# Performance work log

Measured on AMD Instinct MI355X. Metric: run time of the kernel, lower is better.

The kernel has to match this reference:

```python
import jax, jax.numpy as jnp
import numpy as np

B, L, D = 2, 2048, 768
HID = 32           # saliency gate hidden dim
WINDOWS = (8, 32)  # sorted window sizes
CLAMP_MIN, CLAMP_MAX = 0.05, 0.95
SCALE = 1.0 / np.sqrt(D)  # memory_dim == d_model


def setup_inputs() -> dict:
    key = jax.random.key(0)
    ks = jax.random.split(key, 16)
    s = 0.02
    return {
        "hidden_states": jax.random.normal(ks[0], (B, L, D), jnp.float32),
        "saliency_scores": jax.random.uniform(ks[1], (B, L), jnp.float32),
        # SaliencyGate MLP: Linear(1->HID), SiLU, Linear(HID->D)
        "gw1": jax.random.normal(ks[2], (HID, 1), jnp.float32) * s,
        "gb1": jnp.zeros((HID,), jnp.float32),
        "gw2": jax.random.normal(ks[3], (D, HID), jnp.float32) * s,
        "gb2": jnp.zeros((D,), jnp.float32),
        # SelectiveMemory projections
        "wq": jax.random.normal(ks[4], (D, D), jnp.float32) * s,
        "bq": jnp.zeros((D,), jnp.float32),
        "wk": jax.random.normal(ks[5], (D, D), jnp.float32) * s,
        "bk": jnp.zeros((D,), jnp.float32),
        "wv": jax.random.normal(ks[6], (D, D), jnp.float32) * s,
        "bv": jnp.zeros((D,), jnp.float32),
        "wo": jax.random.normal(ks[7], (D, D), jnp.float32) * s,
        "bo": jnp.zeros((D,), jnp.float32),
    }


def _forward(hidden_states, saliency_scores, gw1, gb1, gw2, gb2,
             wq, bq, wk, bk, wv, bv, wo, bo):
    # ---- SaliencyGate: scalar score -> MLP -> sigmoid gate -> clamp ----
    s = saliency_scores[..., None]                          # (b, l, 1)
    h1 = jax.nn.silu(s @ gw1.T + gb1)                       # (b, l, HID)
    gates = jax.nn.sigmoid(h1 @ gw2.T + gb2)                # (b, l, D)
    gates = jnp.clip(gates, CLAMP_MIN, CLAMP_MAX)
    h = hidden_states * gates

    # ---- SelectiveMemory: multi-window local attention ----
    q = h @ wq.T + bq                                       # (b, l, D)
    k = h @ wk.T + bk
    v = h @ wv.T + bv
    # Torch pads hidden_states with zeros before k/v projection; linear of a
    # zero row equals the bias, so padded key/value rows are exactly bk / bv.
    contexts = []
    for w in WINDOWS:
        kp = jnp.concatenate(
            [jnp.broadcast_to(bk, (B, w - 1, D)), k], axis=1)  # (b, l+w-1, D)
        vp = jnp.concatenate(
            [jnp.broadcast_to(bv, (B, w - 1, D)), v], axis=1)
        idx = jnp.arange(L)[:, None] + jnp.arange(w)[None, :]  # (l, w)
        kw = kp[:, idx]                                        # (b, l, w, D)
        vw = vp[:, idx]
        scores = jnp.einsum('bld,blwd->blw', q, kw) * SCALE
        attn = jax.nn.softmax(scores, axis=-1)
        contexts.append(jnp.einsum('blw,blwd->bld', attn, vw))
    merged = (contexts[0] + contexts[1]) * 0.5 if len(contexts) > 1 else contexts[0]
    return h + merged @ wo.T + bo


def reference(hidden_states, saliency_scores, gw1, gb1, gw2, gb2,
              wq, bq, wk, bk, wv, bv, wo, bo):
    return _forward(hidden_states, saliency_scores, gw1, gb1, gw2, gb2,
                    wq, bq, wk, bk, wv, bv, wo, bo)
```

## Files before the change

kernel.cpp:

```cpp
#include <hip/hip_runtime.h>
#include <hip/hip_bf16.h>
#include <stdint.h>

#define Bb 2
#define Ll 2048
#define Dd 768
#define HID 32
#define BL (Bb*Ll)
#define KPAD 32
#define KROWS (KPAD+Ll+16)

typedef __hip_bfloat16 bf16;
typedef __attribute__((ext_vector_type(8))) short short8;
typedef __attribute__((ext_vector_type(4))) short short4s;
typedef __attribute__((ext_vector_type(4))) float floatx4;

__device__ __forceinline__ float b2f(short u) {
    union { float f; unsigned i; } x; x.i = ((unsigned)(unsigned short)u) << 16; return x.f;
}
__device__ __forceinline__ bf16 f2b(float x) { return __float2bfloat16(x); }
__device__ __forceinline__ short f2bs(float x) {
    bf16 t = __float2bfloat16(x);
    union { bf16 h; short s; } u; u.h = t; return u.s;
}

typedef __attribute__((address_space(1))) const unsigned int guint;
typedef __attribute__((address_space(3))) unsigned int luint;
__device__ __forceinline__ void gload16(const bf16* g, bf16* l) {
    __builtin_amdgcn_global_load_lds((guint*)g, (luint*)l, 16, 0, 0);
}

#define CONV_BLOCKS 2304
#define KP_BLOCKS   (Bb*48)
#define VT_BLOCKS   ((Bb*Dd*48)/256)
#define TR_BLOCKS   96
__global__ void prep_kernel(const float* __restrict__ wq, const float* __restrict__ wk,
                            const float* __restrict__ wv, const float* __restrict__ wo,
                            const float* __restrict__ bk, const float* __restrict__ bv,
                            const float* __restrict__ gw2,
                            bf16* __restrict__ wout, bf16* __restrict__ kp, bf16* __restrict__ vT,
                            float* __restrict__ gw2T) {
    int bx = blockIdx.x;
    if (bx < CONV_BLOCKS) {
        int idx = bx * 256 + threadIdx.x;
        const int per = Dd * Dd / 4;
        int w = idx / per, r = idx % per;
        const float* src = (w == 0) ? wq : (w == 1) ? wk : (w == 2) ? wv : wo;
        float4 v = reinterpret_cast<const float4*>(src)[r];
        bf16* o = wout + (size_t)w * Dd * Dd + (size_t)r * 4;
        o[0] = f2b(v.x); o[1] = f2b(v.y); o[2] = f2b(v.z); o[3] = f2b(v.w);
    } else if (bx < CONV_BLOCKS + KP_BLOCKS) {
        int pb = bx - CONV_BLOCKS;
        int b = pb / 48, c = pb % 48;
        int row = (c < 32) ? c : (KPAD + Ll + (c - 32));
        size_t base = ((size_t)b * KROWS + row) * Dd;
        for (int i = threadIdx.x; i < Dd; i += 256)
            kp[base + i] = (c < 32) ? f2b(bk[i]) : f2b(0.f);
    } else if (bx < CONV_BLOCKS + KP_BLOCKS + VT_BLOCKS) {
        int o = (bx - CONV_BLOCKS - KP_BLOCKS) * 256 + threadIdx.x;
        int b = o / (Dd * 48); int rem = o - b * Dd * 48;
        int n = rem / 48, c = rem % 48;
        int col = (c < 32) ? c : (KPAD + Ll + (c - 32));
        vT[((size_t)b * Dd + n) * KROWS + col] = (c < 32) ? f2b(bv[n]) : f2b(0.f);
    } else {
        int o = (bx - CONV_BLOCKS - KP_BLOCKS - VT_BLOCKS) * 256 + threadIdx.x;
        int j = o / Dd, d = o - j * Dd;
        gw2T[o] = gw2[d * HID + j];
    }
}

__global__ __launch_bounds__(256) void gate_kernel(
        const float* __restrict__ hidden, const float* __restrict__ sal,
        const float* __restrict__ gw1, const float* __restrict__ gb1,
        const float* __restrict__ gw2T, const float* __restrict__ gb2,
        bf16* __restrict__ h_b) {
    __shared__ float h1s[8][HID];
    int row0 = blockIdx.x * 8;
    int t = threadIdx.x;
    {
        int rr = t >> 5, j = t & 31;
        float s = sal[row0 + rr];
        float x = s * gw1[j] + gb1[j];
        h1s[rr][j] = x / (1.f + __expf(-x));
    }
    __syncthreads();
#pragma unroll
    for (int dl = 0; dl < 3; ++dl) {
        int d = t + dl * 256;
        float base = gb2[d];
        float acc[8];
#pragma unroll
        for (int rr = 0; rr < 8; ++rr) acc[rr] = base;
#pragma unroll
        for (int j = 0; j < HID; ++j) {
            float wj = gw2T[j * Dd + d];
#pragma unroll
            for (int rr = 0; rr < 8; ++rr) acc[rr] += h1s[rr][j] * wj;
        }
#pragma unroll
        for (int rr = 0; rr < 8; ++rr) {
            float g = 1.f / (1.f + __expf(-acc[rr]));
            g = fminf(fmaxf(g, 0.05f), 0.95f);
            size_t off = (size_t)(row0 + rr) * Dd + d;
            h_b[off] = f2b(hidden[off] * g);
        }
    }
}

template<int NF>
__device__ __forceinline__ void gemm_core(const bf16* __restrict__ Ag, const bf16* __restrict__ Wg,
                                          int m0, int n0, bf16* As, bf16* Bs,
                                          floatx4 (&acc)[4][NF]) {
    const int tid  = threadIdx.x;
    const int wave = tid >> 6, lane = tid & 63;
    const int lrow = lane & 15, koff = (lane >> 4) * 8;
    const int wm = (wave >> 1) * 64, wn = (wave & 1) * (NF * 16);
    const char* Asb = (const char*)As;
    const char* Bsb = (const char*)Bs;

    for (int k0 = 0; k0 < Dd; k0 += 64) {
#pragma unroll
        for (int c = 0; c < 4; ++c) {
            int p = tid * 16 + c * 4096;
            int r = p >> 7;
            int o = (p & 127) ^ ((r & 7) << 4);
            gload16(Ag + (size_t)(m0 + r) * Dd + k0 + (o >> 1),
                    As + (wave * 1024 + c * 4096) / 2);
        }
#pragma unroll
        for (int c = 0; c < NF; ++c) {
            int p = tid * 16 + c * 4096;
            int r = p >> 7;
            int o = (p & 127) ^ ((r & 7) << 4);
            gload16(Wg + (size_t)(n0 + r) * Dd + k0 + (o >> 1),
                    Bs + (wave * 1024 + c * 4096) / 2);
        }
        __syncthreads();
#pragma unroll
        for (int kk = 0; kk < 64; kk += 32) {
            short8 a[4], b[NF];
#pragma unroll
            for (int i = 0; i < 4; ++i) {
                int row = wm + i * 16 + lrow;
                int byt = (row << 7) + (((kk + koff) * 2) ^ ((row & 7) << 4));
                a[i] = *reinterpret_cast<const short8*>(Asb + byt);
            }
#pragma unroll
            for (int j = 0; j < NF; ++j) {
                int row = wn + j * 16 + lrow;
                int byt = (row << 7) + (((kk + koff) * 2) ^ ((row & 7) << 4));
                b[j] = *reinterpret_cast<const short8*>(Bsb + byt);
            }
#pragma unroll
            for (int i = 0; i < 4; ++i)
#pragma unroll
                for (int j = 0; j < NF; ++j)
                    acc[i][j] = __builtin_amdgcn_mfma_f32_16x16x32_bf16(a[i], b[j], acc[i][j], 0, 0, 0);
        }
        __syncthreads();
    }
}

__global__ __launch_bounds__(256) void gemm_qkv(
        const bf16* __restrict__ A, const bf16* __restrict__ W3,
        const float* __restrict__ bq, const float* __restrict__ bk, const float* __restrict__ bv,
        bf16* __restrict__ qo, bf16* __restrict__ kp, bf16* __restrict__ vT) {
    __shared__ bf16 As[128 * 64];
    __shared__ bf16 Bs[128 * 64];
    int bid = blockIdx.x;
    int xcd = bid & 7, idx = bid >> 3;
    int mtile = (xcd >> 1) * 8 + (idx & 7);
    int ntile = (xcd & 1) * 9 + (idx >> 3);
    int tgt = ntile / 6;
    int n0 = (ntile % 6) * 128;
    int m0 = mtile * 128;
    const bf16* W = W3 + (size_t)tgt * Dd * Dd;
    const float* bias = (tgt == 0) ? bq : (tgt == 1) ? bk : bv;

    floatx4 acc[4][4] = {};
    gemm_core<4>(A, W, m0, n0, As, Bs, acc);

    int wave = threadIdx.x >> 6, lane = threadIdx.x & 63;
    int wm = (wave >> 1) * 64, wn = (wave & 1) * 64;
    int crow = (lane >> 4) * 4, ccol = lane & 15;
#pragma unroll
    for (int i = 0; i < 4; ++i)
#pragma unroll
        for (int j = 0; j < 4; ++j) {
            int n = n0 + wn + j * 16 + ccol;
            float bb = bias[n];
            int m = m0 + wm + i * 16 + crow;
            int b_ = m >> 11, l = m & 2047;
            if (tgt == 2) {
                short4s pk;
#pragma unroll
                for (int rr = 0; rr < 4; ++rr) pk[rr] = f2bs(acc[i][j][rr] + bb);
                *reinterpret_cast<short4s*>(vT + ((size_t)b_ * Dd + n) * KROWS + KPAD + l) = pk;
            } else {
#pragma unroll
                for (int rr = 0; rr < 4; ++rr) {
                    size_t orow = (tgt == 0) ? (size_t)(m + rr)
                                             : ((size_t)b_ * KROWS + KPAD + l + rr);
                    bf16* out = (tgt == 0) ? qo : kp;
                    out[orow * Dd + n] = f2b(acc[i][j][rr] + bb);
                }
            }
        }
}

__global__ __launch_bounds__(256) void gemm_out(
        const bf16* __restrict__ A, const bf16* __restrict__ W,
        const float* __restrict__ bias, const bf16* __restrict__ addend,
        float* __restrict__ out) {
    __shared__ bf16 As[128 * 64];
    __shared__ bf16 Bs[64 * 64];
    int bid = blockIdx.x;
    int xcd = bid & 7, idx = bid >> 3;
    int mtile = (xcd >> 1) * 8 + (idx & 7);
    int ntile = (xcd & 1) * 6 + (idx >> 3);
    int n0 = ntile * 64, m0 = mtile * 128;

    floatx4 acc[4][2] = {};
    gemm_core<2>(A, W, m0, n0, As, Bs, acc);

    int wave = threadIdx.x >> 6, lane = threadIdx.x & 63;
    int wm = (wave >> 1) * 64, wn = (wave & 1) * 32;
    int crow = (lane >> 4) * 4, ccol = lane & 15;
#pragma unroll
    for (int i = 0; i < 4; ++i)
#pragma unroll
        for (int j = 0; j < 2; ++j) {
            int n = n0 + wn + j * 16 + ccol;
            float bb = bias[n];
#pragma unroll
            for (int rr = 0; rr < 4; ++rr) {
                int m = m0 + wm + i * 16 + crow + rr;
                size_t o = (size_t)m * Dd + n;
                out[o] = acc[i][j][rr] + bb + b2f(*(const short*)(addend + o));
            }
        }
}

__global__ __launch_bounds__(64) void attn_kernel(
        const bf16* __restrict__ q, const bf16* __restrict__ kp, const bf16* __restrict__ vT,
        bf16* __restrict__ merged) {
    __shared__ bf16 wlds[16 * 64];
    const int lane = threadIdx.x;
    const int bid = blockIdx.x;
    const int g = (bid & 7) * 32 + (bid >> 3);
    const int b = g >> 7, L0 = (g & 127) * 16;
    const int lrow = lane & 15, koff = (lane >> 4) * 8;
    const int crow = (lane >> 4) * 4, ccol = lane & 15;
    const float scale = 0.03608439182435161f;

    const bf16* qbase = q  + ((size_t)(b * Ll + L0 + lrow)) * Dd + koff;
    const bf16* kbase = kp + ((size_t)b * KROWS + L0 + lrow) * Dd + koff;
    floatx4 s[4] = {};
    for (int ks = 0; ks < 24; ++ks) {
        short8 a = *reinterpret_cast<const short8*>(qbase + ks * 32);
#pragma unroll
        for (int f = 0; f < 4; ++f) {
            short8 bb = *reinterpret_cast<const short8*>(kbase + (size_t)f * 16 * Dd + ks * 32);
            s[f] = __builtin_amdgcn_mfma_f32_16x16x32_bf16(a, bb, s[f], 0, 0, 0);
        }
    }

#pragma unroll
    for (int rr = 0; rr < 4; ++rr) {
        int r = crow + rr;
        float z[4], e[4];
#pragma unroll
        for (int f = 0; f < 4; ++f) {
            int j = f * 16 + ccol;
            bool valid = (j >= r + 1) && (j <= r + 32);
            z[f] = valid ? s[f][rr] * scale : -3.0e38f;
        }
        float m = fmaxf(fmaxf(z[0], z[1]), fmaxf(z[2], z[3]));
#pragma unroll
        for (int off = 1; off < 16; off <<= 1) m = fmaxf(m, __shfl_xor(m, off));
        float S32 = 0.f, S8 = 0.f;
#pragma unroll
        for (int f = 0; f < 4; ++f) {
            e[f] = __expf(z[f] - m);
            S32 += e[f];
            int j = f * 16 + ccol;
            S8 += ((j >= r + 25) && (j <= r + 32)) ? e[f] : 0.f;
        }
#pragma unroll
        for (int off = 1; off < 16; off <<= 1) {
            S32 += __shfl_xor(S32, off);
            S8  += __shfl_xor(S8, off);
        }
        float i32 = 0.5f / S32, i8 = 0.5f / S8;
#pragma unroll
        for (int f = 0; f < 4; ++f) {
            int j = f * 16 + ccol;
            float w = e[f] * i32 + (((j >= r + 25) && (j <= r + 32)) ? e[f] * i8 : 0.f);
            int byt = ((r * 64 + j) * 2) ^ ((r & 7) << 4);
            *reinterpret_cast<bf16*>(reinterpret_cast<char*>(wlds) + byt) = f2b(w);
        }
    }
    __syncthreads();

    short8 wa[2];
#pragma unroll
    for (int ks = 0; ks < 2; ++ks) {
        int byt = ((lrow * 64 + ks * 32 + koff) * 2) ^ ((lrow & 7) << 4);
        wa[ks] = *reinterpret_cast<const short8*>(reinterpret_cast<const char*>(wlds) + byt);
    }
    const bf16* vbase = vT + (size_t)b * Dd * KROWS + L0;
    bf16* obase = merged + ((size_t)(b * Ll + L0 + ccol)) * Dd;
    for (int c = 0; c < 6; ++c) {
#pragma unroll
        for (int fn = 0; fn < 8; ++fn) {
            int nr = c * 128 + fn * 16;
            floatx4 acc = {};
#pragma unroll
            for (int ks = 0; ks < 2; ++ks) {
                short8 bb = *reinterpret_cast<const short8*>(vbase + (size_t)(nr + lrow) * KROWS + ks * 32 + koff);
                acc = __builtin_amdgcn_mfma_f32_16x16x32_bf16(bb, wa[ks], acc, 0, 0, 0);
            }
            short4s pk;
#pragma unroll
            for (int rr = 0; rr < 4; ++rr) pk[rr] = f2bs(acc[rr]);
            *reinterpret_cast<short4s*>(obase + nr + crow) = pk;
        }
    }
}

extern "C" void kernel_launch(void* const* d_in, const int* in_sizes, int n_in,
                              void* d_out, int out_size, void* d_ws, size_t ws_size,
                              hipStream_t stream) {
    const float* hidden = (const float*)d_in[0];
    const float* sal    = (const float*)d_in[1];
    const float* gw1    = (const float*)d_in[2];
    const float* gb1    = (const float*)d_in[3];
    const float* gw2    = (const float*)d_in[4];
    const float* gb2    = (const float*)d_in[5];
    const float* wq     = (const float*)d_in[6];
    const float* bq     = (const float*)d_in[7];
    const float* wk     = (const float*)d_in[8];
    const float* bk     = (const float*)d_in[9];
    const float* wv     = (const float*)d_in[10];
    const float* bv     = (const float*)d_in[11];
    const float* wo     = (const float*)d_in[12];
    const float* bo     = (const float*)d_in[13];
    float* out = (float*)d_out;

    const size_t nBL  = (size_t)BL * Dd;
    const size_t nPad = (size_t)Bb * KROWS * Dd;
    char* p = (char*)d_ws;
    bf16* h_b = (bf16*)p; p += nBL * 2;
    bf16* q_b = (bf16*)p; p += nBL * 2;
    bf16* kpd = (bf16*)p; p += nPad * 2;
    bf16* vT  = (bf16*)p; p += nPad * 2;
    bf16* m_b = (bf16*)p; p += nBL * 2;
    bf16* w_b = (bf16*)p; p += (size_t)4 * Dd * Dd * 2;
    float* g2T = (float*)p; p += (size_t)HID * Dd * 4;

    prep_kernel<<<dim3(CONV_BLOCKS + KP_BLOCKS + VT_BLOCKS + TR_BLOCKS), 256, 0, stream>>>(
        wq, wk, wv, wo, bk, bv, gw2, w_b, kpd, vT, g2T);
    gate_kernel<<<dim3(BL / 8), 256, 0, stream>>>(hidden, sal, gw1, gb1, g2T, gb2, h_b);
    gemm_qkv<<<dim3(576), 256, 0, stream>>>(h_b, w_b, bq, bk, bv, q_b, kpd, vT);
    attn_kernel<<<dim3(256), 64, 0, stream>>>(q_b, kpd, vT, m_b);
    gemm_out<<<dim3(384), 256, 0, stream>>>(m_b, w_b + (size_t)3 * Dd * Dd, bo, h_b, out);
}
```

Measured before the change: 84.26 us.

## Fuse prep and gate kernels, widen QKV GEMM K-tile to 128

Merges the weight-conversion/padding prep kernel with the saliency gate kernel into one launch. Each gate block now transposes gw2 into shared memory as bf16 itself, so the separate transpose pass and the global gw2T buffer are gone. The QKV GEMM uses a 128-wide K tile, which halves its loop iterations and barriers but doubles its shared memory, and both GEMMs get a two-blocks-per-CU launch bound. Every gate block re-reads all of gw2 and uses a 49KB shared array, which can lower occupancy for the whole fused kernel, including the cheap prep blocks.

```diff
diff --git a/kernel.cpp b/kernel.cpp
--- a/kernel.cpp
+++ b/kernel.cpp
@@ -30,84 +30,88 @@
     __builtin_amdgcn_global_load_lds((guint*)g, (luint*)l, 16, 0, 0);
 }
 
-#define CONV_BLOCKS 2304
-#define KP_BLOCKS   (Bb*48)
-#define VT_BLOCKS   ((Bb*Dd*48)/256)
-#define TR_BLOCKS   96
-__global__ void prep_kernel(const float* __restrict__ wq, const float* __restrict__ wk,
-                            const float* __restrict__ wv, const float* __restrict__ wo,
-                            const float* __restrict__ bk, const float* __restrict__ bv,
-                            const float* __restrict__ gw2,
-                            bf16* __restrict__ wout, bf16* __restrict__ kp, bf16* __restrict__ vT,
-                            float* __restrict__ gw2T) {
-    int bx = blockIdx.x;
-    if (bx < CONV_BLOCKS) {
-        int idx = bx * 256 + threadIdx.x;
+#define CONV_VB 2304
+#define KP_VB   (Bb*48)
+#define VT_VB   ((Bb*Dd*48)/256)
+#define PREP_VB (CONV_VB+KP_VB+VT_VB)
+#define GATE_VB (BL/8)
+__global__ __launch_bounds__(256) void prep_gate_kernel(
+        const float* __restrict__ wq, const float* __restrict__ wk,
+        const float* __restrict__ wv, const float* __restrict__ wo,
+        const float* __restrict__ bk, const float* __restrict__ bv,
+        const float* __restrict__ hidden, const float* __restrict__ sal,
+        const float* __restrict__ gw1, const float* __restrict__ gb1,
+        const float* __restrict__ gw2, const float* __restrict__ gb2,
+        bf16* __restrict__ wout, bf16* __restrict__ kp, bf16* __restrict__ vT,
+        bf16* __restrict__ h_b) {
+    __shared__ bf16 g2t[32 * 770];
+    __shared__ float h1s[8][HID];
+    int bx = blockIdx.x, tid = threadIdx.x;
+    if (bx < CONV_VB) {
+        int idx = bx * 256 + tid;
         const int per = Dd * Dd / 4;
         int w = idx / per, r = idx % per;
         const float* src = (w == 0) ? wq : (w == 1) ? wk : (w == 2) ? wv : wo;
         float4 v = reinterpret_cast<const float4*>(src)[r];
         bf16* o = wout + (size_t)w * Dd * Dd + (size_t)r * 4;
         o[0] = f2b(v.x); o[1] = f2b(v.y); o[2] = f2b(v.z); o[3] = f2b(v.w);
-    } else if (bx < CONV_BLOCKS + KP_BLOCKS) {
-        int pb = bx - CONV_BLOCKS;
+    } else if (bx < CONV_VB + KP_VB) {
+        int pb = bx - CONV_VB;
         int b = pb / 48, c = pb % 48;
         int row = (c < 32) ? c : (KPAD + Ll + (c - 32));
         size_t base = ((size_t)b * KROWS + row) * Dd;
-        for (int i = threadIdx.x; i < Dd; i += 256)
+        for (int i = tid; i < Dd; i += 256)
             kp[base + i] = (c < 32) ? f2b(bk[i]) : f2b(0.f);
-    } else if (bx < CONV_BLOCKS + KP_BLOCKS + VT_BLOCKS) {
-        int o = (bx - CONV_BLOCKS - KP_BLOCKS) * 256 + threadIdx.x;
+    } else if (bx < PREP_VB) {
+        int o = (bx - CONV_VB - KP_VB) * 256 + tid;
         int b = o / (Dd * 48); int rem = o - b * Dd * 48;
         int n = rem / 48, c = rem % 48;
         int col = (c < 32) ? c : (KPAD + Ll + (c - 32));
         vT[((size_t)b * Dd + n) * KROWS + col] = (c < 32) ? f2b(bv[n]) : f2b(0.f);
     } else {
-        int o = (bx - CONV_BLOCKS - KP_BLOCKS - VT_BLOCKS) * 256 + threadIdx.x;
-        int j = o / Dd, d = o - j * Dd;
-        gw2T[o] = gw2[d * HID + j];
-    }
-}
-
-__global__ __launch_bounds__(256) void gate_kernel(
-        const float* __restrict__ hidden, const float* __restrict__ sal,
-        const float* __restrict__ gw1, const float* __restrict__ gb1,
-        const float* __restrict__ gw2T, const float* __restrict__ gb2,
-        bf16* __restrict__ h_b) {
-    __shared__ float h1s[8][HID];
-    int row0 = blockIdx.x * 8;
-    int t = threadIdx.x;
-    {
-        int rr = t >> 5, j = t & 31;
-        float s = sal[row0 + rr];
-        float x = s * gw1[j] + gb1[j];
-        h1s[rr][j] = x / (1.f + __expf(-x));
-    }
-    __syncthreads();
-#pragma unroll
-    for (int dl = 0; dl < 3; ++dl) {
-        int d = t + dl * 256;
-        float base = gb2[d];
-        float acc[8];
-#pragma unroll
-        for (int rr = 0; rr < 8; ++rr) acc[rr] = base;
-#pragma unroll
-        for (int j = 0; j < HID; ++j) {
-            float wj = gw2T[j * Dd + d];
-#pragma unroll
-            for (int rr = 0; rr < 8; ++rr) acc[rr] += h1s[rr][j] * wj;
-        }
-#pragma unroll
-        for (int rr = 0; rr < 8; ++rr) {
-            float g = 1.f / (1.f + __expf(-acc[rr]));
-            g = fminf(fmaxf(g, 0.05f), 0.95f);
-            size_t off = (size_t)(row0 + rr) * Dd + d;
-            h_b[off] = f2b(hidden[off] * g);
-        }
-    }
-}
-
-template<int NF>
+        int row0 = (bx - PREP_VB) * 8;
+#pragma unroll
+        for (int k2 = 0; k2 < 24; ++k2) {
+            int o4 = tid + k2 * 256;
+            float4 v = reinterpret_cast<const float4*>(gw2)[o4];
+            int d = o4 >> 3, j = (o4 & 7) * 4;
+            g2t[(j + 0) * 770 + d] = f2b(v.x);
+            g2t[(j + 1) * 770 + d] = f2b(v.y);
+            g2t[(j + 2) * 770 + d] = f2b(v.z);
+            g2t[(j + 3) * 770 + d] = f2b(v.w);
+        }
+        {
+            int rr = tid >> 5, j = tid & 31;
+            float s = sal[row0 + rr];
+            float x = s * gw1[j] + gb1[j];
+            h1s[rr][j] = x / (1.f + __expf(-x));
+        }
+        __syncthreads();
+#pragma unroll
+        for (int dl = 0; dl < 3; ++dl) {
+            int d = tid + dl * 256;
+            float base = gb2[d];
+            float acc[8];
+#pragma unroll
+            for (int rr = 0; rr < 8; ++rr) acc[rr] = base;
+#pragma unroll
+            for (int j = 0; j < HID; ++j) {
+                float wj = b2f(*(const short*)&g2t[j * 770 + d]);
+#pragma unroll
+                for (int rr = 0; rr < 8; ++rr) acc[rr] += h1s[rr][j] * wj;
+            }
+#pragma unroll
+            for (int rr = 0; rr < 8; ++rr) {
+                float g = 1.f / (1.f + __expf(-acc[rr]));
+                g = fminf(fmaxf(g, 0.05f), 0.95f);
+                size_t off = (size_t)(row0 + rr) * Dd + d;
+                h_b[off] = f2b(hidden[off] * g);
+            }
+        }
+    }
+}
+
+template<int NF, int BK>
 __device__ __forceinline__ void gemm_core(const bf16* __restrict__ Ag, const bf16* __restrict__ Wg,
                                           int m0, int n0, bf16* As, bf16* Bs,
                                           floatx4 (&acc)[4][NF]) {
@@ -115,40 +119,41 @@
     const int wave = tid >> 6, lane = tid & 63;
     const int lrow = lane & 15, koff = (lane >> 4) * 8;
     const int wm = (wave >> 1) * 64, wn = (wave & 1) * (NF * 16);
+    const int RS = BK * 2;
     const char* Asb = (const char*)As;
     const char* Bsb = (const char*)Bs;
 
-    for (int k0 = 0; k0 < Dd; k0 += 64) {
-#pragma unroll
-        for (int c = 0; c < 4; ++c) {
+    for (int k0 = 0; k0 < Dd; k0 += BK) {
+#pragma unroll
+        for (int c = 0; c < BK / 16; ++c) {
             int p = tid * 16 + c * 4096;
-            int r = p >> 7;
-            int o = (p & 127) ^ ((r & 7) << 4);
+            int r = p / RS;
+            int o = (p % RS) ^ ((r & 7) << 4);
             gload16(Ag + (size_t)(m0 + r) * Dd + k0 + (o >> 1),
                     As + (wave * 1024 + c * 4096) / 2);
         }
 #pragma unroll
-        for (int c = 0; c < NF; ++c) {
+        for (int c = 0; c < NF * BK / 64; ++c) {
             int p = tid * 16 + c * 4096;
-            int r = p >> 7;
-            int o = (p & 127) ^ ((r & 7) << 4);
+            int r = p / RS;
+            int o = (p % RS) ^ ((r & 7) << 4);
             gload16(Wg + (size_t)(n0 + r) * Dd + k0 + (o >> 1),
                     Bs + (wave * 1024 + c * 4096) / 2);
         }
         __syncthreads();
 #pragma unroll
-        for (int kk = 0; kk < 64; kk += 32) {
+        for (int kk = 0; kk < BK; kk += 32) {
             short8 a[4], b[NF];
 #pragma unroll
             for (int i = 0; i < 4; ++i) {
                 int row = wm + i * 16 + lrow;
-                int byt = (row << 7) + (((kk + koff) * 2) ^ ((row & 7) << 4));
+                int byt = row * RS + (((kk + koff) * 2) ^ ((row & 7) << 4));
                 a[i] = *reinterpret_cast<const short8*>(Asb + byt);
             }
 #pragma unroll
             for (int j = 0; j < NF; ++j) {
                 int row = wn + j * 16 + lrow;
-                int byt = (row << 7) + (((kk + koff) * 2) ^ ((row & 7) << 4));
+                int byt = row * RS + (((kk + koff) * 2) ^ ((row & 7) << 4));
                 b[j] = *reinterpret_cast<const short8*>(Bsb + byt);
             }
 #pragma unroll
@@ -161,12 +166,12 @@
     }
 }
 
-__global__ __launch_bounds__(256) void gemm_qkv(
+__global__ __launch_bounds__(256, 2) void gemm_qkv(
         const bf16* __restrict__ A, const bf16* __restrict__ W3,
         const float* __restrict__ bq, const float* __restrict__ bk, const float* __restrict__ bv,
         bf16* __restrict__ qo, bf16* __restrict__ kp, bf16* __restrict__ vT) {
-    __shared__ bf16 As[128 * 64];
-    __shared__ bf16 Bs[128 * 64];
+    __shared__ bf16 As[128 * 128];
+    __shared__ bf16 Bs[128 * 128];
     int bid = blockIdx.x;
     int xcd = bid & 7, idx = bid >> 3;
     int mtile = (xcd >> 1) * 8 + (idx & 7);
@@ -178,7 +183,7 @@
     const float* bias = (tgt == 0) ? bq : (tgt == 1) ? bk : bv;
 
     floatx4 acc[4][4] = {};
-    gemm_core<4>(A, W, m0, n0, As, Bs, acc);
+    gemm_core<4, 128>(A, W, m0, n0, As, Bs, acc);
 
     int wave = threadIdx.x >> 6, lane = threadIdx.x & 63;
     int wm = (wave >> 1) * 64, wn = (wave & 1) * 64;
@@ -201,14 +206,14 @@
                 for (int rr = 0; rr < 4; ++rr) {
                     size_t orow = (tgt == 0) ? (size_t)(m + rr)
                                              : ((size_t)b_ * KROWS + KPAD + l + rr);
-                    bf16* out = (tgt == 0) ? qo : kp;
-                    out[orow * Dd + n] = f2b(acc[i][j][rr] + bb);
+                    bf16* outp = (tgt == 0) ? qo : kp;
+                    outp[orow * Dd + n] = f2b(acc[i][j][rr] + bb);
                 }
             }
         }
 }
 
-__global__ __launch_bounds__(256) void gemm_out(
+__global__ __launch_bounds__(256, 2) void gemm_out(
         const bf16* __restrict__ A, const bf16* __restrict__ W,
         const float* __restrict__ bias, const bf16* __restrict__ addend,
         float* __restrict__ out) {
@@ -221,7 +226,7 @@
     int n0 = ntile * 64, m0 = mtile * 128;
 
     floatx4 acc[4][2] = {};
-    gemm_core<2>(A, W, m0, n0, As, Bs, acc);
+    gemm_core<2, 64>(A, W, m0, n0, As, Bs, acc);
 
     int wave = threadIdx.x >> 6, lane = threadIdx.x & 63;
     int wm = (wave >> 1) * 64, wn = (wave & 1) * 32;
@@ -264,7 +269,6 @@
             s[f] = __builtin_amdgcn_mfma_f32_16x16x32_bf16(a, bb, s[f], 0, 0, 0);
         }
     }
-
 #pragma unroll
     for (int rr = 0; rr < 4; ++rr) {
         int r = crow + rr;
@@ -295,9 +299,9 @@
 #pragma unroll
         for (int f = 0; f < 4; ++f) {
             int j = f * 16 + ccol;
-            float w = e[f] * i32 + (((j >= r + 25) && (j <= r + 32)) ? e[f] * i8 : 0.f);
+            float wgt = e[f] * i32 + (((j >= r + 25) && (j <= r + 32)) ? e[f] * i8 : 0.f);
             int byt = ((r * 64 + j) * 2) ^ ((r & 7) << 4);
-            *reinterpret_cast<bf16*>(reinterpret_cast<char*>(wlds) + byt) = f2b(w);
+            *reinterpret_cast<bf16*>(reinterpret_cast<char*>(wlds) + byt) = f2b(wgt);
         }
     }
     __syncthreads();
@@ -356,11 +360,9 @@
     bf16* vT  = (bf16*)p; p += nPad * 2;
     bf16* m_b = (bf16*)p; p += nBL * 2;
     bf16* w_b = (bf16*)p; p += (size_t)4 * Dd * Dd * 2;
-    float* g2T = (float*)p; p += (size_t)HID * Dd * 4;
-
-    prep_kernel<<<dim3(CONV_BLOCKS + KP_BLOCKS + VT_BLOCKS + TR_BLOCKS), 256, 0, stream>>>(
-        wq, wk, wv, wo, bk, bv, gw2, w_b, kpd, vT, g2T);
-    gate_kernel<<<dim3(BL / 8), 256, 0, stream>>>(hidden, sal, gw1, gb1, g2T, gb2, h_b);
+
+    prep_gate_kernel<<<dim3(PREP_VB + GATE_VB), 256, 0, stream>>>(
+        wq, wk, wv, wo, bk, bv, hidden, sal, gw1, gb1, gw2, gb2, w_b, kpd, vT, h_b);
     gemm_qkv<<<dim3(576), 256, 0, stream>>>(h_b, w_b, bq, bk, bv, q_b, kpd, vT);
     attn_kernel<<<dim3(256), 64, 0, stream>>>(q_b, kpd, vT, m_b);
     gemm_out<<<dim3(384), 256, 0, stream>>>(m_b, w_b + (size_t)3 * Dd * Dd, bo, h_b, out);
```

After: 79.68 us. 1.06x faster.
